# Kernel optimization log

Measured on AMD Instinct MI355X. Metric: run time of the kernel, lower is better.

## Reference

```python
import jax, jax.numpy as jnp
import numpy as np

EPS = 1e-5  # norm_eps


def setup_inputs() -> dict:
    key = jax.random.key(0)
    ks = jax.random.split(key, 9)
    N, C, T, H, W = 2, 1024, 8, 28, 28
    Di = 512
    s = 0.02  # weight init scale
    return {
        "x": jax.random.normal(ks[0], (N, C, T, H, W), jnp.float32),
        "w_theta": jax.random.normal(ks[1], (Di, C), jnp.float32) * s,
        "b_theta": jax.random.normal(ks[2], (Di,), jnp.float32) * s,
        "w_phi": jax.random.normal(ks[3], (Di, C), jnp.float32) * s,
        "b_phi": jax.random.normal(ks[4], (Di,), jnp.float32) * s,
        "w_g": jax.random.normal(ks[5], (Di, C), jnp.float32) * s,
        "b_g": jax.random.normal(ks[6], (Di,), jnp.float32) * s,
        "w_out": jax.random.normal(ks[7], (C, Di), jnp.float32) * s,
        "b_out": jax.random.normal(ks[8], (C,), jnp.float32) * s,
    }


def reference(x, w_theta, b_theta, w_phi, b_phi, w_g, b_g, w_out, b_out):
    # ProgressNL forward at step==0 (y == x), pool_size=None,
    # instantiation='softmax', norm_type='layernorm' (GroupNorm(1, C, affine=False)).
    N, C, T, H, W = x.shape
    Di = w_theta.shape[0]
    xf = x.reshape(N, C, T * H * W)  # flatten spatio-temporal tokens

    # 1x1x1 convs == per-token matmuls
    theta = jnp.einsum('dc,nct->ndt', w_theta, xf) + b_theta[None, :, None]  # [N,Di,THW]
    phi = jnp.einsum('dc,nct->ndt', w_phi, xf) + b_phi[None, :, None]
    g = jnp.einsum('dc,nct->ndt', w_g, xf) + b_g[None, :, None]

    # attention: softmax(theta^T phi / sqrt(Di)) @ g^T
    scores = jnp.einsum('nct,ncp->ntp', theta, phi) * (Di ** -0.5)  # [N,THW,THW]
    attn = jax.nn.softmax(scores, axis=-1)
    o = jnp.einsum('ntp,ncp->nct', attn, g)  # [N,Di,THW]

    # output 1x1x1 conv
    p = jnp.einsum('cd,ndt->nct', w_out, o) + b_out[None, :, None]  # [N,C,THW]

    # GroupNorm(1, C, affine=False): normalize over (C,T,H,W) per sample
    mean = jnp.mean(p, axis=(1, 2), keepdims=True)
    var = jnp.var(p, axis=(1, 2), keepdims=True)
    p = (p - mean) * jax.lax.rsqrt(var + EPS)

    return x + p.reshape(N, C, T, H, W)
```

## Files before the change

### kernel.cpp

```cpp
#include <hip/hip_runtime.h>

typedef _Float16 f16x8 __attribute__((ext_vector_type(8)));
typedef _Float16 f16x4 __attribute__((ext_vector_type(4)));
typedef float    f32x4 __attribute__((ext_vector_type(4)));

#define THW 6272
#define CCH 1024
#define DI  512

__device__ __forceinline__ void gload16(const _Float16* g, _Float16* l)
{
    __builtin_amdgcn_global_load_lds(
        (const __attribute__((address_space(1))) void*)g,
        (__attribute__((address_space(3))) void*)l, 16, 0, 0);
}

template<typename OUT_T, int BM, bool BIAS_M, bool BIAS_N, bool EXPP, bool GNP, bool RSC>
__global__ __launch_bounds__(256, 4)
void gemm_nt(const _Float16* __restrict__ A, size_t lda, size_t sAn,
             const _Float16* __restrict__ Bt, size_t ldb, size_t sBn,
             OUT_T* __restrict__ C, size_t ldc, size_t sCn,
             int K, int Kfull, float alpha,
             const float* __restrict__ bias_m,
             const float* __restrict__ bias_n,
             float* __restrict__ psum,
             const float* __restrict__ row_scale,
             int rows_ps,
             int gx, int gy)
{
    constexpr int MF = BM / 32;
    __shared__ _Float16 As[BM * 64];
    __shared__ _Float16 Bs[128 * 64];
    __shared__ float rs[4], rs2[4];
    const int tid  = threadIdx.x;
    const int lane = tid & 63;
    const int wave = tid >> 6;
    const int wr = wave >> 1, wc = wave & 1;

    const int nwg = gridDim.x;
    const int q = nwg >> 3, rr = nwg & 7;
    const int xcd = blockIdx.x & 7, seq = blockIdx.x >> 3;
    const int wg = (xcd < rr ? xcd * (q + 1) : rr * (q + 1) + (xcd - rr) * q) + seq;
    const int zz  = wg / (gx * gy);
    const int rem = wg - zz * gx * gy;
    const int by  = rem / gx, bx = rem - by * gx;
    const int n   = zz & 1;
    const int ks  = zz >> 1;

    const int koff = ks * K;
    const int klen = (Kfull - koff < K) ? (Kfull - koff) : K;

    A  += (size_t)n * sAn + (size_t)by * BM * lda + koff;
    Bt += (size_t)n * sBn + (size_t)bx * 128 * ldb + koff;

    const int srow = lane >> 3, sk = (lane & 7) * 8;
    const _Float16* gA = A  + (size_t)(wave * (MF * 8) + srow) * lda + sk;
    const _Float16* gB = Bt + (size_t)(wave * 32 + srow) * ldb + sk;
    _Float16* lA = As + wave * (MF * 512) + lane * 8;
    _Float16* lB = Bs + wave * 2048 + lane * 8;

    const int r  = lane & 15;
    const int kg = lane >> 4;

    f32x4 acc[MF][4] = {};

    for (int kt = 0; kt < klen; kt += 64) {
#pragma unroll
        for (int i = 0; i < MF; i++)
            gload16(gA + (size_t)(i * 8) * lda, lA + i * 512);
#pragma unroll
        for (int i = 0; i < 4; i++)
            gload16(gB + (size_t)(i * 8) * ldb, lB + i * 512);
        gA += 64; gB += 64;
        __syncthreads();
#pragma unroll
        for (int kk = 0; kk < 2; kk++) {
            f16x8 af[MF], bf[4];
#pragma unroll
            for (int mf = 0; mf < MF; mf++)
                af[mf] = *(const f16x8*)(As + (wr * (BM / 2) + mf * 16 + r) * 64 + kk * 32 + kg * 8);
#pragma unroll
            for (int nf = 0; nf < 4; nf++)
                bf[nf] = *(const f16x8*)(Bs + (wc * 64 + nf * 16 + r) * 64 + kk * 32 + kg * 8);
#pragma unroll
            for (int mf = 0; mf < MF; mf++)
#pragma unroll
                for (int nf = 0; nf < 4; nf++)
                    acc[mf][nf] = __builtin_amdgcn_mfma_f32_16x16x32_f16(
                        af[mf], bf[nf], acc[mf][nf], 0, 0, 0);
        }
        __syncthreads();
    }

    C += (size_t)zz * sCn;
    float gs = 0.f, gs2 = 0.f;

#pragma unroll
    for (int mf = 0; mf < MF; mf++) {
#pragma unroll
        for (int qi = 0; qi < 4; qi++) {
            size_t row = (size_t)by * BM + wr * (BM / 2) + mf * 16 + kg * 4 + qi;
            float bm = BIAS_M ? bias_m[row] : 0.f;
            float sc = RSC ? row_scale[(size_t)n * rows_ps + row] : 1.f;
            float rsum = 0.f;
#pragma unroll
            for (int nf = 0; nf < 4; nf++) {
                size_t col = (size_t)bx * 128 + wc * 64 + nf * 16 + r;
                float val = acc[mf][nf][qi] * alpha + bm + (BIAS_N ? bias_n[col] : 0.f);
                if (EXPP) { val = __expf(val); rsum += val; }
                else if (RSC) val *= sc;
                if (GNP) { gs += val; gs2 += val * val; }
                C[row * ldc + col] = (OUT_T)val;
            }
            if (EXPP) {
                rsum += __shfl_xor(rsum, 1);
                rsum += __shfl_xor(rsum, 2);
                rsum += __shfl_xor(rsum, 4);
                rsum += __shfl_xor(rsum, 8);
                if (r == 0)
                    psum[((size_t)n * rows_ps + row) * 98 + bx * 2 + wc] = rsum;
            }
        }
    }
    if (GNP) {
        for (int o = 32; o; o >>= 1) {
            gs  += __shfl_xor(gs, o);
            gs2 += __shfl_xor(gs2, o);
        }
        if (lane == 0) { rs[wave] = gs; rs2[wave] = gs2; }
        __syncthreads();
        if (tid == 0) {
            psum[(size_t)wg * 2]     = rs[0] + rs[1] + rs[2] + rs[3];
            psum[(size_t)wg * 2 + 1] = rs2[0] + rs2[1] + rs2[2] + rs2[3];
        }
    }
}

__global__ __launch_bounds__(256)
void rowsum_inv(const float* __restrict__ psum, float* __restrict__ inv, int nrows)
{
    int rI = blockIdx.x * 256 + threadIdx.x;
    if (rI < nrows) {
        const float* p = psum + (size_t)rI * 98;
        float s = 0.f;
#pragma unroll 7
        for (int i = 0; i < 98; i++) s += p[i];
        inv[rI] = 1.f / s;
    }
}

__global__ __launch_bounds__(256)
void combine4(const _Float16* __restrict__ Op, _Float16* __restrict__ Ot,
              int tr, int t0)
{
    const int per_n8 = tr * 64;
    int idx = blockIdx.x * 256 + threadIdx.x;
    if (idx >= 2 * per_n8) return;
    int n = idx / per_n8;
    int rem = idx - n * per_n8;
    int t = rem >> 6, d8 = rem & 63;
    const size_t slice = (size_t)tr * 512;
    float o[8] = {};
#pragma unroll
    for (int ks = 0; ks < 4; ks++) {
        f16x8 v = *(const f16x8*)(Op + (size_t)(ks * 2 + n) * slice + (size_t)rem * 8);
#pragma unroll
        for (int j = 0; j < 8; j++) o[j] += (float)v[j];
    }
    f16x8 w;
#pragma unroll
    for (int j = 0; j < 8; j++) w[j] = (_Float16)o[j];
    *(f16x8*)(Ot + ((size_t)(n * THW + t0 + t) * DI + d8 * 8)) = w;
}

__global__ __launch_bounds__(256)
void pack_weights(const float* __restrict__ wt, const float* __restrict__ wp,
                  const float* __restrict__ wg, const float* __restrict__ wo,
                  const float* __restrict__ bt, const float* __restrict__ bp,
                  _Float16* __restrict__ Wtp, _Float16* __restrict__ Wg,
                  _Float16* __restrict__ Wo, float* __restrict__ btp)
{
    int i = blockIdx.x * 256 + threadIdx.x;
    if (i < 512 * 1024) {
        Wtp[i]              = (_Float16)wt[i];
        Wtp[i + 512 * 1024] = (_Float16)wp[i];
        Wg[i]               = (_Float16)wg[i];
        Wo[i]               = (_Float16)wo[i];
    }
    if (i < 512) { btp[i] = bt[i]; btp[i + 512] = bp[i]; }
}

__global__ __launch_bounds__(256)
void transpose_cast(const float* __restrict__ x, _Float16* __restrict__ xT)
{
    __shared__ float tile[64][65];
    const int n  = blockIdx.z;
    const int t0 = blockIdx.x * 64;
    const int c0 = blockIdx.y * 64;
    const int tid = threadIdx.x;
    const float* xp = x + ((size_t)n * CCH + c0) * THW + t0;
#pragma unroll
    for (int i = 0; i < 16; i++) {
        int v = tid + i * 256;
        int c = v >> 6, t = v & 63;
        tile[t][c] = xp[(size_t)c * THW + t];
    }
    __syncthreads();
    _Float16* op = xT + ((size_t)n * THW + t0) * CCH + c0;
#pragma unroll
    for (int i = 0; i < 2; i++) {
        int v = tid + i * 256;
        int t = v >> 3, c8 = (v & 7) * 8;
        f16x8 o;
#pragma unroll
        for (int j = 0; j < 8; j++) o[j] = (_Float16)tile[t][c8 + j];
        *(f16x8*)(op + (size_t)t * CCH + c8) = o;
    }
}

__global__ __launch_bounds__(256)
void reduce_final(const float* __restrict__ partials, float* __restrict__ stats, int nblk)
{
    const int n = blockIdx.x;
    float s = 0.f, s2 = 0.f;
    for (int i = threadIdx.x; i < nblk; i += 256) {
        s  += partials[((size_t)n * nblk + i) * 2];
        s2 += partials[((size_t)n * nblk + i) * 2 + 1];
    }
    for (int o = 32; o; o >>= 1) { s += __shfl_xor(s, o); s2 += __shfl_xor(s2, o); }
    __shared__ float rs[4], rs2[4];
    if ((threadIdx.x & 63) == 0) { rs[threadIdx.x >> 6] = s; rs2[threadIdx.x >> 6] = s2; }
    __syncthreads();
    if (threadIdx.x == 0) {
        float S1 = rs[0] + rs[1] + rs[2] + rs[3];
        float S2 = rs2[0] + rs2[1] + rs2[2] + rs2[3];
        const float invc = 1.f / ((float)CCH * (float)THW);
        float mean = S1 * invc;
        float var  = S2 * invc - mean * mean;
        stats[n * 2]     = mean;
        stats[n * 2 + 1] = rsqrtf(var + 1e-5f);
    }
}

__global__ __launch_bounds__(256)
void final_residual(const float* __restrict__ x, float* __restrict__ pc_out,
                    const float* __restrict__ stats, size_t total4)
{
    const size_t per_n4 = (size_t)CCH * THW / 4;
    for (size_t i = (size_t)blockIdx.x * 256 + threadIdx.x; i < total4;
         i += (size_t)gridDim.x * 256) {
        int n = (int)(i / per_n4);
        float mean = stats[n * 2], rstd = stats[n * 2 + 1];
        f32x4 xv = ((const f32x4*)x)[i];
        f32x4 pv = ((f32x4*)pc_out)[i];
        f32x4 ov;
#pragma unroll
        for (int j = 0; j < 4; j++) ov[j] = xv[j] + (pv[j] - mean) * rstd;
        ((f32x4*)pc_out)[i] = ov;
    }
}

extern "C" void kernel_launch(void* const* d_in, const int* in_sizes, int n_in,
                              void* d_out, int out_size, void* d_ws, size_t ws_size,
                              hipStream_t stream)
{
    const float* x  = (const float*)d_in[0];
    const float* wt = (const float*)d_in[1];
    const float* bt = (const float*)d_in[2];
    const float* wp = (const float*)d_in[3];
    const float* bp = (const float*)d_in[4];
    const float* wg = (const float*)d_in[5];
    const float* bg = (const float*)d_in[6];
    const float* wo = (const float*)d_in[7];
    const float* bo = (const float*)d_in[8];
    float* out = (float*)d_out;

    char* ws = (char*)d_ws;
    size_t off = 0;
    auto alloc = [&](size_t b) -> void* {
        off = (off + 255) & ~(size_t)255;
        void* p = ws + off;
        off += b;
        return p;
    };

    _Float16* Wtp = (_Float16*)alloc((size_t)1024 * 1024 * 2);
    _Float16* Wg  = (_Float16*)alloc((size_t)512 * 1024 * 2);
    _Float16* Wo  = (_Float16*)alloc((size_t)1024 * 512 * 2);
    float*    btp = (float*)alloc(1024 * 4);
    _Float16* xT  = (_Float16*)alloc((size_t)2 * THW * CCH * 2);
    _Float16* tpg = (_Float16*)alloc((size_t)2 * THW * 1024 * 2);
    _Float16* g   = (_Float16*)alloc((size_t)2 * DI * THW * 2);
    _Float16* Ot  = (_Float16*)alloc((size_t)2 * THW * DI * 2);
    float*    gnp   = (float*)alloc((size_t)1568 * 2 * 4);
    float*    stats = (float*)alloc(4 * 4);

    const size_t tile_bytes = (size_t)2 * 128 * (THW * 2 + 98 * 4 + 4);
    size_t avail = (ws_size > off + 256) ? ws_size - off - 256 : 0;
    int tiles_fit = (int)(avail / tile_bytes);
    if (tiles_fit < 1) tiles_fit = 1;
    if (tiles_fit > 49) tiles_fit = 49;
    int nch = (49 + tiles_fit - 1) / tiles_fit;
    int tpc = (49 + nch - 1) / nch;

    _Float16* S    = (_Float16*)alloc((size_t)2 * tpc * 128 * THW * 2);
    float*    psum = (float*)alloc((size_t)2 * tpc * 128 * 98 * 4);
    float*    inv  = (float*)alloc((size_t)2 * tpc * 128 * 4);
    _Float16* Opart = (_Float16*)out;

    const size_t sXT = (size_t)THW * CCH;
    const size_t sG  = (size_t)DI * THW;

    pack_weights<<<2048, 256, 0, stream>>>(wt, wp, wg, wo, bt, bp, Wtp, Wg, Wo, btp);
    transpose_cast<<<dim3(THW / 64, CCH / 64, 2), 256, 0, stream>>>(x, xT);

    gemm_nt<_Float16, 128, false, true, false, false, false><<<8 * 49 * 2, 256, 0, stream>>>(
        xT, CCH, sXT, Wtp, CCH, 0, tpg, 1024, sXT, CCH, CCH, 1.f,
        nullptr, btp, nullptr, nullptr, 0, 8, 49);

    gemm_nt<_Float16, 64, true, false, false, false, false><<<49 * 8 * 2, 256, 0, stream>>>(
        Wg, CCH, 0, xT, CCH, sXT, g, THW, sG, CCH, CCH, 1.f,
        bg, nullptr, nullptr, nullptr, 0, 49, 8);

    const float scale = 0.044194173824159216f;
    for (int ch = 0; ch < nch; ch++) {
        int tile0 = ch * tpc;
        int tiles = (49 - tile0 < tpc) ? (49 - tile0) : tpc;
        size_t t0 = (size_t)tile0 * 128;
        int tchRows = tiles * 128;

        gemm_nt<_Float16, 128, false, false, true, false, false><<<49 * tiles * 2, 256, 0, stream>>>(
            tpg + t0 * 1024, 1024, sXT, tpg + 512, 1024, sXT,
            S, THW, (size_t)tchRows * THW, DI, DI, scale,
            nullptr, nullptr, psum, nullptr, tchRows, 49, tiles);

        rowsum_inv<<<(2 * tchRows + 255) / 256, 256, 0, stream>>>(psum, inv, 2 * tchRows);

        gemm_nt<_Float16, 128, false, false, false, false, true><<<4 * tiles * 8, 256, 0, stream>>>(
            S, THW, (size_t)tchRows * THW, g, THW, sG,
            Opart, DI, (size_t)tchRows * DI, 1600, THW, 1.f,
            nullptr, nullptr, nullptr, inv, tchRows, 4, tiles);

        combine4<<<(tchRows * 128 + 255) / 256, 256, 0, stream>>>(
            Opart, Ot, tchRows, (int)t0);
    }

    gemm_nt<float, 128, true, false, false, true, false><<<49 * 8 * 2, 256, 0, stream>>>(
        Wo, DI, 0, Ot, DI, sG, out, THW, (size_t)CCH * THW, DI, DI, 1.f,
        bo, nullptr, gnp, nullptr, 0, 49, 8);

    reduce_final<<<2, 256, 0, stream>>>(gnp, stats, 392);
    final_residual<<<2048, 256, 0, stream>>>(x, out, stats, (size_t)2 * CCH * THW / 4);
}
```

Before: 388.3 us.

## Swizzle score GEMM tiles into 7x7 supertiles and store output projection in fp16

The score GEMM now maps workgroups onto 7x7 supertiles so that neighbouring blocks share A and B panels in L2. The output-projection GEMM writes fp16 into the reused tpg buffer instead of fp32 into out, and the final residual kernel reads that fp16 data and writes fp32 to out. Together these cut L2 misses and the HBM traffic of the final pass. The fp16 intermediate adds rounding error before the GroupNorm.

```diff
diff --git a/kernel.cpp b/kernel.cpp
--- a/kernel.cpp
+++ b/kernel.cpp
@@ -25,7 +25,7 @@
              const float* __restrict__ bias_n,
              float* __restrict__ psum,
              const float* __restrict__ row_scale,
-             int rows_ps,
+             int rows_ps, int stile,
              int gx, int gy)
 {
     constexpr int MF = BM / 32;
@@ -43,7 +43,18 @@
     const int wg = (xcd < rr ? xcd * (q + 1) : rr * (q + 1) + (xcd - rr) * q) + seq;
     const int zz  = wg / (gx * gy);
     const int rem = wg - zz * gx * gy;
-    const int by  = rem / gx, bx = rem - by * gx;
+    int by, bx;
+    if (stile > 0) {
+        const int per = stile * stile;
+        const int sgx = gx / stile;
+        const int sid = rem / per, wi = rem - sid * per;
+        const int srow = sid / sgx, scol = sid - srow * sgx;
+        const int wrow = wi / stile;
+        by = srow * stile + wrow;
+        bx = scol * stile + (wi - wrow * stile);
+    } else {
+        by = rem / gx; bx = rem - by * gx;
+    }
     const int n   = zz & 1;
     const int ks  = zz >> 1;
 
@@ -243,8 +254,9 @@
 }
 
 __global__ __launch_bounds__(256)
-void final_residual(const float* __restrict__ x, float* __restrict__ pc_out,
-                    const float* __restrict__ stats, size_t total4)
+void final_residual(const float* __restrict__ x, const _Float16* __restrict__ pc16,
+                    float* __restrict__ outp, const float* __restrict__ stats,
+                    size_t total4)
 {
     const size_t per_n4 = (size_t)CCH * THW / 4;
     for (size_t i = (size_t)blockIdx.x * 256 + threadIdx.x; i < total4;
@@ -252,11 +264,11 @@
         int n = (int)(i / per_n4);
         float mean = stats[n * 2], rstd = stats[n * 2 + 1];
         f32x4 xv = ((const f32x4*)x)[i];
-        f32x4 pv = ((f32x4*)pc_out)[i];
+        f16x4 pv = ((const f16x4*)pc16)[i];
         f32x4 ov;
 #pragma unroll
-        for (int j = 0; j < 4; j++) ov[j] = xv[j] + (pv[j] - mean) * rstd;
-        ((f32x4*)pc_out)[i] = ov;
+        for (int j = 0; j < 4; j++) ov[j] = xv[j] + ((float)pv[j] - mean) * rstd;
+        ((f32x4*)outp)[i] = ov;
     }
 }
 
@@ -307,6 +319,7 @@
     float*    psum = (float*)alloc((size_t)2 * tpc * 128 * 98 * 4);
     float*    inv  = (float*)alloc((size_t)2 * tpc * 128 * 4);
     _Float16* Opart = (_Float16*)out;
+    _Float16* Pc16  = tpg;
 
     const size_t sXT = (size_t)THW * CCH;
     const size_t sG  = (size_t)DI * THW;
@@ -316,11 +329,11 @@
 
     gemm_nt<_Float16, 128, false, true, false, false, false><<<8 * 49 * 2, 256, 0, stream>>>(
         xT, CCH, sXT, Wtp, CCH, 0, tpg, 1024, sXT, CCH, CCH, 1.f,
-        nullptr, btp, nullptr, nullptr, 0, 8, 49);
+        nullptr, btp, nullptr, nullptr, 0, 0, 8, 49);
 
     gemm_nt<_Float16, 64, true, false, false, false, false><<<49 * 8 * 2, 256, 0, stream>>>(
         Wg, CCH, 0, xT, CCH, sXT, g, THW, sG, CCH, CCH, 1.f,
-        bg, nullptr, nullptr, nullptr, 0, 49, 8);
+        bg, nullptr, nullptr, nullptr, 0, 0, 49, 8);
 
     const float scale = 0.044194173824159216f;
     for (int ch = 0; ch < nch; ch++) {
@@ -328,27 +341,28 @@
         int tiles = (49 - tile0 < tpc) ? (49 - tile0) : tpc;
         size_t t0 = (size_t)tile0 * 128;
         int tchRows = tiles * 128;
+        int stile = (tiles % 7 == 0) ? 7 : 0;
 
         gemm_nt<_Float16, 128, false, false, true, false, false><<<49 * tiles * 2, 256, 0, stream>>>(
             tpg + t0 * 1024, 1024, sXT, tpg + 512, 1024, sXT,
             S, THW, (size_t)tchRows * THW, DI, DI, scale,
-            nullptr, nullptr, psum, nullptr, tchRows, 49, tiles);
+            nullptr, nullptr, psum, nullptr, tchRows, stile, 49, tiles);
 
         rowsum_inv<<<(2 * tchRows + 255) / 256, 256, 0, stream>>>(psum, inv, 2 * tchRows);
 
         gemm_nt<_Float16, 128, false, false, false, false, true><<<4 * tiles * 8, 256, 0, stream>>>(
             S, THW, (size_t)tchRows * THW, g, THW, sG,
             Opart, DI, (size_t)tchRows * DI, 1600, THW, 1.f,
-            nullptr, nullptr, nullptr, inv, tchRows, 4, tiles);
+            nullptr, nullptr, nullptr, inv, tchRows, 0, 4, tiles);
 
         combine4<<<(tchRows * 128 + 255) / 256, 256, 0, stream>>>(
             Opart, Ot, tchRows, (int)t0);
     }
 
-    gemm_nt<float, 128, true, false, false, true, false><<<49 * 8 * 2, 256, 0, stream>>>(
-        Wo, DI, 0, Ot, DI, sG, out, THW, (size_t)CCH * THW, DI, DI, 1.f,
-        bo, nullptr, gnp, nullptr, 0, 49, 8);
+    gemm_nt<_Float16, 128, true, false, false, true, false><<<49 * 8 * 2, 256, 0, stream>>>(
+        Wo, DI, 0, Ot, DI, sG, Pc16, THW, (size_t)CCH * THW, DI, DI, 1.f,
+        bo, nullptr, gnp, nullptr, 0, 0, 49, 8);
 
     reduce_final<<<2, 256, 0, stream>>>(gnp, stats, 392);
-    final_residual<<<2048, 256, 0, stream>>>(x, out, stats, (size_t)2 * CCH * THW / 4);
-}
+    final_residual<<<2048, 256, 0, stream>>>(x, Pc16, out, stats, (size_t)2 * CCH * THW / 4);
+}
```

After: 381.0 us. About the same (-1.9%).
